# Optimization experiments

Hardware: AMD Instinct MI355X
Metric: run time of the kernel (lower is better)

## Reference

```python
import jax, jax.numpy as jnp
import numpy as np
from jax import lax

D_MODEL=1024; D_STATE=128; D_CONV=4; EXPAND=2; HEADDIM=64
D_INNER=EXPAND*D_MODEL; NHEADS=D_INNER//HEADDIM
POOL=64; SUMDIM=256; TAU1=0.5; TAU2=0.4

def rmsnorm(x, w, eps):
    return x * lax.rsqrt(jnp.mean(x*x, axis=-1, keepdims=True) + eps) * w

def silu(x):
    return x * jax.nn.sigmoid(x)

def setup_inputs():
    key = jax.random.key(0)
    ks = jax.random.split(key, 20)
    B, T = 4, 2048
    d_in_proj = 2*D_INNER + 2*D_STATE + NHEADS
    inp = {
        'x': jax.random.normal(ks[0], (B, T, D_MODEL), jnp.float32),
        'pool': jnp.zeros((B, POOL, SUMDIM), jnp.float32),
        'priorities': jnp.zeros((B, POOL), jnp.float32),
        'counts': jnp.zeros((B,), jnp.int32),
        'norm_w': jnp.ones((D_MODEL,), jnp.float32),
        'in_w': jax.random.normal(ks[1], (d_in_proj, D_MODEL), jnp.float32)*0.02,
        'conv_w': jax.random.normal(ks[2], (D_INNER+2*D_STATE, 1, D_CONV), jnp.float32)*0.1,
        'conv_b': jnp.zeros((D_INNER+2*D_STATE,), jnp.float32),
        'dt_bias': jax.random.uniform(ks[3], (NHEADS,), jnp.float32, -5.0, -1.0),
        'A_log': jnp.log(jax.random.uniform(ks[4], (NHEADS,), jnp.float32, 1.0, 16.0)),
        'Dp': jax.random.normal(ks[5], (NHEADS,), jnp.float32)*0.1 + 1.0,
        'ssm_norm_w': jnp.ones((D_INNER,), jnp.float32),
        'out_w': jax.random.normal(ks[6], (D_MODEL, D_INNER), jnp.float32)*0.02,
        'score_w1': jax.random.normal(ks[7], (D_MODEL//4, D_MODEL), jnp.float32)*0.03,
        'score_w2': jax.random.normal(ks[8], (1, D_MODEL//4), jnp.float32)*0.06,
        'summ_w': jax.random.normal(ks[9], (SUMDIM, D_MODEL), jnp.float32)*0.03,
        'q_w': jax.random.normal(ks[10], (SUMDIM, D_MODEL), jnp.float32)*0.03,
        'k_w': jax.random.normal(ks[11], (SUMDIM, SUMDIM), jnp.float32)*0.06,
        'v_w': jax.random.normal(ks[12], (D_MODEL, SUMDIM), jnp.float32)*0.06,
        'gate_w': jax.random.normal(ks[13], (D_MODEL, 2*D_MODEL), jnp.float32)*0.02,
    }
    return inp

def mamba2(u, in_w, conv_w, conv_b, dt_bias, A_log, Dp, ssm_norm_w, out_w):
    B, T, _ = u.shape
    zxbcdt = u @ in_w.T                      # [B,T,2*d_inner+2*d_state+nheads]
    z = zxbcdt[..., :D_INNER]
    xBC = zxbcdt[..., D_INNER:2*D_INNER+2*D_STATE]
    dt = jax.nn.softplus(zxbcdt[..., 2*D_INNER+2*D_STATE:] + dt_bias)  # [B,T,H]
    # causal depthwise conv over time
    xc = jnp.transpose(xBC, (0, 2, 1))       # [B,C,T]
    xc = lax.conv_general_dilated(xc, conv_w, (1,), [(D_CONV-1, 0)],
                                  dimension_numbers=('NCH', 'OIH', 'NCH'),
                                  feature_group_count=D_INNER+2*D_STATE)
    xBC = silu(jnp.transpose(xc + conv_b[None, :, None], (0, 2, 1)))
    xh = xBC[..., :D_INNER].reshape(B, T, NHEADS, HEADDIM)
    Bm = xBC[..., D_INNER:D_INNER+D_STATE]   # [B,T,N]
    Cm = xBC[..., D_INNER+D_STATE:]          # [B,T,N]
    A = -jnp.exp(A_log)                      # [H]
    dA = jnp.exp(dt * A)                     # [B,T,H]
    def step(h, inp):
        dA_t, dt_t, x_t, B_t, C_t = inp      # [B,H],[B,H],[B,H,P],[B,N],[B,N]
        h = dA_t[:, :, None, None]*h + (dt_t[:, :, None]*x_t)[..., None]*B_t[:, None, None, :]
        y = jnp.einsum('bhpn,bn->bhp', h, C_t)
        return h, y
    h0 = jnp.zeros((B, NHEADS, HEADDIM, D_STATE), u.dtype)
    xs = (jnp.swapaxes(dA, 0, 1), jnp.swapaxes(dt, 0, 1), jnp.swapaxes(xh, 0, 1),
          jnp.swapaxes(Bm, 0, 1), jnp.swapaxes(Cm, 0, 1))
    _, ys = lax.scan(step, h0, xs)           # [T,B,H,P]
    y = jnp.swapaxes(ys, 0, 1) + Dp[None, None, :, None]*xh
    y = y.reshape(B, T, D_INNER)
    y = rmsnorm(y * silu(z), ssm_norm_w, 1e-5)
    return y @ out_w.T

def pool_update(tokens, scores, pool, priorities, counts,
                summ_w):
    B, T, D = tokens.shape
    mask = scores > TAU1
    order = jnp.argsort(-scores, axis=1)     # descending
    s_scores = jnp.take_along_axis(scores, order, 1)
    s_tokens = jnp.take_along_axis(tokens, order[..., None], 1)
    s_mask = jnp.take_along_axis(mask, order, 1)
    summaries = s_tokens @ summ_w.T          # [B,T,SUMDIM]
    nslots = min(T, POOL)
    bidx = jnp.arange(B)
    def slot_step(carry, inp):
        pool, pri, counts = carry
        has_imp, imp, summ = inp             # [B],[B],[B,SUMDIM]
        add = has_imp & (counts < POOL)
        widx = jnp.minimum(counts, POOL-1)
        pool = pool.at[bidx, widx].set(jnp.where(add[:, None], summ, pool[bidx, widx]))
        pri = pri.at[bidx, widx].set(jnp.where(add, imp, pri[bidx, widx]))
        counts = counts + add.astype(counts.dtype)
        replace = has_imp & (counts >= POOL)
        min_idx = jnp.argmin(pri, axis=1)
        min_p = pri[bidx, min_idx]
        should = replace & (imp > min_p)
        pool = pool.at[bidx, min_idx].set(jnp.where(should[:, None], summ, pool[bidx, min_idx]))
        pri = pri.at[bidx, min_idx].set(jnp.where(should, imp, pri[bidx, min_idx]))
        return (pool, pri, counts), None
    xs = (jnp.swapaxes(s_mask[:, :nslots], 0, 1),
          jnp.swapaxes(s_scores[:, :nslots], 0, 1),
          jnp.swapaxes(summaries[:, :nslots], 0, 1))
    (pool, priorities, counts), _ = lax.scan(slot_step, (pool, priorities, counts), xs)
    return pool, priorities, counts

def reference(x, pool, priorities, counts, norm_w, in_w, conv_w, conv_b, dt_bias,
              A_log, Dp, ssm_norm_w, out_w, score_w1, score_w2, summ_w,
              q_w, k_w, v_w, gate_w):
    B = x.shape[0]
    y = x + mamba2(rmsnorm(x, norm_w, 1e-4), in_w, conv_w, conv_b, dt_bias,
                   A_log, Dp, ssm_norm_w, out_w)
    scores = jax.nn.sigmoid(jnp.maximum(y @ score_w1.T, 0.0) @ score_w2.T)[..., 0]
    # layer_idx % cross_layer_frequency == 0 -> update path taken
    pool, priorities, counts = pool_update(y, scores, pool, priorities, counts, summ_w)
    mask = jnp.arange(POOL)[None, :] < counts[:, None]
    q = y @ q_w.T                            # [B,T,S]
    k = pool @ k_w.T                         # [B,P,S]
    v = pool @ v_w.T                         # [B,P,D]
    attn = jnp.einsum('bts,bps->btp', q, k) / (SUMDIM ** 0.5)
    attn = jnp.where(mask[:, None, :], attn, -jnp.inf)
    attn = jnp.nan_to_num(jax.nn.softmax(attn, axis=-1), nan=0.0)
    retrieved = jnp.einsum('btp,bpd->btd', attn, v)
    gate = jax.nn.sigmoid(jnp.concatenate([y, retrieved], axis=-1) @ gate_w.T)
    rmask = ((jnp.mean(scores, axis=1) > TAU2) & (counts > 0)).astype(y.dtype)[:, None, None]
    y = y + gate * retrieved * rmask
    return (y, pool, priorities, counts)
```

## Files before the change

kernel.cpp:

```cpp
#include <hip/hip_runtime.h>


using u16 = unsigned short;
using f16x8 = __attribute__((ext_vector_type(8))) _Float16;
using f32x4  = __attribute__((ext_vector_type(4))) float;

#define DEV __device__ __forceinline__

#define GLOAD4(g, l)  __builtin_amdgcn_global_load_lds((const __attribute__((address_space(1))) void*)(g), (__attribute__((address_space(3))) void*)(l), 4, 0, 0)
#define GLOAD16(g, l) __builtin_amdgcn_global_load_lds((const __attribute__((address_space(1))) void*)(g), (__attribute__((address_space(3))) void*)(l), 16, 0, 0)
#define VMWAIT(N) asm volatile("s_waitcnt vmcnt(" #N ")" ::: "memory")

static constexpr int Bb = 4, T = 2048, D = 1024;
static constexpr int DIN = 2048, DST = 128, NH = 32;
static constexpr int DPROJ = 4384;
static constexpr int CCH = 2304;
static constexpr int ROWS = Bb * T;
static constexpr int NC = 4, CL = 512;
static constexpr float RSC = 4096.f, RSCI = 1.f / 4096.f;

DEV u16 f2h_bits(float f) { union { _Float16 h; u16 u; } v; v.h = (_Float16)f; return v.u; }
DEV float h2f(u16 u) { union { _Float16 h; u16 u; } v; v.u = u; return (float)v.h; }
DEV double sigd(double x) { return 1.0 / (1.0 + exp(-x)); }
DEV int swz(int c) { return c ^ ((c >> 3) & 3); }

__global__ void diag_kernel(float* o, float v) { if (threadIdx.x == 0) o[0] = v; }
__global__ void zerod_kernel(double* p, int n) { if ((int)threadIdx.x < n) p[threadIdx.x] = 0.0; }

__global__ void split2_kernel(const float* __restrict__ in, u16* __restrict__ out, long n) {
    long i = (long)blockIdx.x * 256 + threadIdx.x;
    if (i >= n) return;
    float v = in[i];
    u16 h = f2h_bits(v);
    float r1 = (v - h2f(h)) * RSC;
    out[i] = h;
    out[n + i] = f2h_bits(r1);
}

__global__ __launch_bounds__(256) void rms_x_kernel(const float* __restrict__ x, const float* __restrict__ w,
                                                    u16* __restrict__ up, long pstride) {
    long row = blockIdx.x; int tid = threadIdx.x;
    const float* xr = x + row * D;
    float4 xv = *(const float4*)(xr + tid * 4);
    double ss = (double)xv.x * xv.x + (double)xv.y * xv.y + (double)xv.z * xv.z + (double)xv.w * xv.w;
    for (int off = 1; off < 64; off <<= 1) ss += __shfl_xor(ss, off);
    __shared__ double tmp[4];
    if ((tid & 63) == 0) tmp[tid >> 6] = ss;
    __syncthreads();
    double tot = tmp[0] + tmp[1] + tmp[2] + tmp[3];
    double scale = 1.0 / sqrt(tot / (double)D + 1e-4);
    float4 wv = *(const float4*)(w + tid * 4);
    long base = row * D + tid * 4;
    float vals[4];
    vals[0] = (float)((double)xv.x * scale * (double)wv.x);
    vals[1] = (float)((double)xv.y * scale * (double)wv.y);
    vals[2] = (float)((double)xv.z * scale * (double)wv.z);
    vals[3] = (float)((double)xv.w * scale * (double)wv.w);
#pragma unroll
    for (int j = 0; j < 4; j++) {
        float f = vals[j];
        u16 h = f2h_bits(f);
        up[base + j] = h;
        up[pstride + base + j] = f2h_bits((f - h2f(h)) * RSC);
    }
}

template <int NP>
DEV void stage_one(u16* s0, u16* s1, const float* __restrict__ src, long ld,
                   int row0, int lastrow, int k0, int tid) {
    int r = tid >> 1, cb = (tid & 1) * 2;
    long rg = row0 + r; if (rg > lastrow) rg = lastrow;
    const float* p = src + rg * ld + k0 + cb * 8;
    u16 h16[16], l16[16];
#pragma unroll
    for (int q = 0; q < 4; q++) {
        float4 v4 = *(const float4*)(p + q * 4);
        float vv[4] = { v4.x, v4.y, v4.z, v4.w };
#pragma unroll
        for (int j = 0; j < 4; j++) {
            float xv = vv[j];
            u16 h = f2h_bits(xv);
            h16[q * 4 + j] = h;
            if constexpr (NP == 2) l16[q * 4 + j] = f2h_bits((xv - h2f(h)) * RSC);
        }
    }
    int o0 = swz(r * 4 + cb) * 8, o1 = swz(r * 4 + cb + 1) * 8;
    *(uint4*)(s0 + o0) = *(const uint4*)(h16);
    *(uint4*)(s0 + o1) = *(const uint4*)(h16 + 8);
    if constexpr (NP == 2) {
        *(uint4*)(s1 + o0) = *(const uint4*)(l16);
        *(uint4*)(s1 + o1) = *(const uint4*)(l16 + 8);
    }
}

DEV void stage_pre_dma(u16* dst, const u16* __restrict__ src, long ld,
                       int row0, int lastrow, int k0, int wid, int lane) {
#pragma unroll
    for (int j = 0; j < 2; j++) {
        int s = wid * 128 + j * 64 + lane;
        int g = swz(s);
        int r = g >> 2, cs = g & 3;
        long rg = row0 + r; if (rg > lastrow) rg = lastrow;
        const u16* gp = src + rg * ld + k0 + cs * 8;
        GLOAD16(gp, dst + (wid * 128 + j * 64) * 8);
    }
}

template <int NP, int MODE, bool BP, bool AP>
__global__ __launch_bounds__(256, 2) void gemm_f32(
    const float* __restrict__ A, long lda,
    const u16* __restrict__ Ap, size_t astride,
    const float* __restrict__ B, long ldb,
    const u16* __restrict__ Bp, size_t bstride,
    int M, int N, int K,
    float* __restrict__ out0, float* __restrict__ out1,
    const float* __restrict__ aux0, const float* __restrict__ aux1,
    float* __restrict__ dtb, float* __restrict__ dab) {
    __shared__ __align__(16) u16 sm[NP * 2 * 4096];
    u16* As[2]; u16* Bs[2];
#pragma unroll
    for (int p = 0; p < NP; p++) { As[p] = sm + p * 4096; Bs[p] = sm + (NP + p) * 4096; }
    int tid = threadIdx.x, lane = tid & 63, wid = tid >> 6;
    int wr = wid >> 1, wc = wid & 1;
    int nwg = gridDim.x * gridDim.y;
    int wg = blockIdx.y * gridDim.x + blockIdx.x;
    int lin = (wg & 7) * (nwg >> 3) + (wg >> 3);
    int tM = (lin / gridDim.x) * 128, tN = (lin % gridDim.x) * 128;

    f32x4 acc1[4][4], acc2[4][4];
#pragma unroll
    for (int i = 0; i < 4; i++)
#pragma unroll
        for (int j = 0; j < 4; j++) {
            acc1[i][j] = f32x4{0.f, 0.f, 0.f, 0.f};
            if constexpr (NP == 2) acc2[i][j] = f32x4{0.f, 0.f, 0.f, 0.f};
        }

    int rA = wr * 64 + (lane & 15);
    int rB = wc * 64 + (lane & 15);
    int kc = lane >> 4;
    int oA[4], oB[4];
#pragma unroll
    for (int i = 0; i < 4; i++) {
        oA[i] = swz((rA + i * 16) * 4 + kc) * 8;
        oB[i] = swz((rB + i * 16) * 4 + kc) * 8;
    }

    int nsteps = K / 32;
    for (int kt = 0; kt < nsteps; ++kt) {
        int k0 = kt * 32;
        __syncthreads();
        if constexpr (BP) {
#pragma unroll
            for (int p = 0; p < NP; p++)
                stage_pre_dma(Bs[p], Bp + (size_t)p * bstride, K, tN, N - 1, k0, wid, lane);
        }
        if constexpr (AP) {
#pragma unroll
            for (int p = 0; p < NP; p++)
                stage_pre_dma(As[p], Ap + (size_t)p * astride, K, tM, M - 1, k0, wid, lane);
        } else {
            stage_one<NP>(As[0], NP == 2 ? As[1] : nullptr, A, lda, tM, M - 1, k0, tid);
        }
        if constexpr (!BP) {
            stage_one<NP>(Bs[0], NP == 2 ? Bs[1] : nullptr, B, ldb, tN, N - 1, k0, tid);
        }
        __syncthreads();
        f16x8 fa[4], fb[4];
#pragma unroll
        for (int i = 0; i < 4; i++) {
            fa[i] = *(const f16x8*)(As[0] + oA[i]);
            fb[i] = *(const f16x8*)(Bs[0] + oB[i]);
        }
#pragma unroll
        for (int mi = 0; mi < 4; mi++)
#pragma unroll
            for (int ni = 0; ni < 4; ni++)
                acc1[mi][ni] = __builtin_amdgcn_mfma_f32_16x16x32_f16(fa[mi], fb[ni], acc1[mi][ni], 0, 0, 0);
        if constexpr (NP == 2) {
#pragma unroll
            for (int i = 0; i < 4; i++) fb[i] = *(const f16x8*)(Bs[1] + oB[i]);
#pragma unroll
            for (int mi = 0; mi < 4; mi++)
#pragma unroll
                for (int ni = 0; ni < 4; ni++)
                    acc2[mi][ni] = __builtin_amdgcn_mfma_f32_16x16x32_f16(fa[mi], fb[ni], acc2[mi][ni], 0, 0, 0);
#pragma unroll
            for (int i = 0; i < 4; i++) {
                fa[i] = *(const f16x8*)(As[1] + oA[i]);
                fb[i] = *(const f16x8*)(Bs[0] + oB[i]);
            }
#pragma unroll
            for (int mi = 0; mi < 4; mi++)
#pragma unroll
                for (int ni = 0; ni < 4; ni++)
                    acc2[mi][ni] = __builtin_amdgcn_mfma_f32_16x16x32_f16(fa[mi], fb[ni], acc2[mi][ni], 0, 0, 0);
        }
    }
    int laneh = lane >> 4, lanel = lane & 15;
#pragma unroll
    for (int mi = 0; mi < 4; mi++)
#pragma unroll
        for (int ni = 0; ni < 4; ni++) {
            int col = tN + wc * 64 + ni * 16 + lanel;
            if (col >= N) continue;
#pragma unroll
            for (int r = 0; r < 4; r++) {
                long row = tM + wr * 64 + mi * 16 + laneh * 4 + r;
                float v = acc1[mi][ni][r];
                if constexpr (NP == 2) v += acc2[mi][ni][r] * RSCI;
                if constexpr (MODE == 0) {
                    if (col < 2048) out0[row * 2048 + col] = v;
                    else if (col < 4352) out1[row * 2304 + (col - 2048)] = v;
                    else {
                        int h = col - 4352;
                        double xx = (double)v + (double)aux0[h];
                        double sp = (xx > 30.0) ? xx : log1p(exp(xx));
                        double a = -exp((double)aux1[h]);
                        dtb[row * NH + h] = (float)sp;
                        dab[row * NH + h] = (float)exp(sp * a);
                    }
                } else if constexpr (MODE == 1) {
                    out0[row * 256 + col] = fmaxf(v, 0.f);
                } else if constexpr (MODE == 2) {
                    float y = aux0[row * 1024 + col] + v;
                    out0[row * 1024 + col] = y;
                    out1[row * 2048 + col] = y;
                } else if constexpr (MODE == 3) {
                    out0[row * 256 + col] = v;
                } else {
                    double g = sigd((double)v);
                    float retr = aux0[row * 2048 + 1024 + col];
                    out0[row * 1024 + col] += (float)(g * (double)retr * (double)aux1[row >> 11]);
                }
            }
        }
}

__global__ __launch_bounds__(256) void conv_kernel(const float* __restrict__ xin, const float* __restrict__ cw,
                                                   const float* __restrict__ cb, float* __restrict__ xbc) {
    int blk = blockIdx.x;
    int ct = blk % 36; int tt = (blk / 36) % 32; int b = blk / (36 * 32);
    int c0 = ct * 64, t0 = tt * 64;
    int tid = threadIdx.x;
    __shared__ float tile[67 * 64];
    for (int i = tid; i < 67 * 64; i += 256) {
        int r = i >> 6, c = i & 63;
        int t = t0 - 3 + r;
        tile[i] = (t >= 0) ? xin[((long)(b * T + t)) * CCH + c0 + c] : 0.f;
    }
    __syncthreads();
    int c = tid & 63; int rb = (tid >> 6) * 16;
    int gc = c0 + c;
    double w0 = cw[gc * 4], w1 = cw[gc * 4 + 1], w2 = cw[gc * 4 + 2], w3 = cw[gc * 4 + 3];
    double bias = cb[gc];
    for (int j = 0; j < 16; j++) {
        int tl = rb + j;
        double a = bias + w0 * (double)tile[tl * 64 + c] + w1 * (double)tile[(tl + 1) * 64 + c]
                        + w2 * (double)tile[(tl + 2) * 64 + c] + w3 * (double)tile[(tl + 3) * 64 + c];
        xbc[((long)(b * T + t0 + tl)) * CCH + gc] = (float)(a * sigd(a));
    }
}

#define SCAN_STEP(tt) do { \
    int slot_ = (tt) & 7; \
    float dtv_ = sdt[(tt)], dav_ = sda[(tt)]; \
    float xt0_ = sx[slot_][pp], xt1_ = sx[slot_][pp + 8]; \
    float dtx0_ = dtv_ * xt0_, dtx1_ = dtv_ * xt1_; \
    const float4* BP_ = (const float4*)&sbc[slot_][0]; \
    float y0a_ = 0.f, y0b_ = 0.f, y1a_ = 0.f, y1b_ = 0.f; \
    _Pragma("unroll") \
    for (int r_ = 0; r_ < 4; r_++) { \
        float4 bv_ = BP_[r_ * 8 + sub]; \
        float4 cv_ = BP_[32 + r_ * 8 + sub]; \
        hs0[r_*4+0] = fmaf(dav_, hs0[r_*4+0], dtx0_ * bv_.x); y0a_ = fmaf(hs0[r_*4+0], cv_.x, y0a_); \
        hs0[r_*4+1] = fmaf(dav_, hs0[r_*4+1], dtx0_ * bv_.y); y0b_ = fmaf(hs0[r_*4+1], cv_.y, y0b_); \
        hs0[r_*4+2] = fmaf(dav_, hs0[r_*4+2], dtx0_ * bv_.z); y0a_ = fmaf(hs0[r_*4+2], cv_.z, y0a_); \
        hs0[r_*4+3] = fmaf(dav_, hs0[r_*4+3], dtx0_ * bv_.w); y0b_ = fmaf(hs0[r_*4+3], cv_.w, y0b_); \
        hs1[r_*4+0] = fmaf(dav_, hs1[r_*4+0], dtx1_ * bv_.x); y1a_ = fmaf(hs1[r_*4+0], cv_.x, y1a_); \
        hs1[r_*4+1] = fmaf(dav_, hs1[r_*4+1], dtx1_ * bv_.y); y1b_ = fmaf(hs1[r_*4+1], cv_.y, y1b_); \
        hs1[r_*4+2] = fmaf(dav_, hs1[r_*4+2], dtx1_ * bv_.z); y1a_ = fmaf(hs1[r_*4+2], cv_.z, y1a_); \
        hs1[r_*4+3] = fmaf(dav_, hs1[r_*4+3], dtx1_ * bv_.w); y1b_ = fmaf(hs1[r_*4+3], cv_.w, y1b_); \
    } \
    float y0_ = y0a_ + y0b_, y1_ = y1a_ + y1b_; \
    y0_ += __shfl_xor(y0_, 1); y0_ += __shfl_xor(y0_, 2); y0_ += __shfl_xor(y0_, 4); \
    y1_ += __shfl_xor(y1_, 1); y1_ += __shfl_xor(y1_, 2); y1_ += __shfl_xor(y1_, 4); \
    if (sub == 0) { \
        yout[(long)(tt) * DIN] = y0_ + sDp * xt0_; \
        yout[(long)(tt) * DIN + 8] = y1_ + sDp * xt1_; \
    } \
    runA *= dav_; \
    if (wrc && l == 0) cumAp[(tt)] = runA; \
} while (0)

#define SCAN_ISSUE(s) do { \
    GLOAD16(bcsrc + (long)(s) * CCH, &sbc[(s) & 7][0]); \
    GLOAD4(xsrc + (long)(s) * CCH, &sx[(s) & 7][0]); \
} while (0)

__global__ __launch_bounds__(64) void scan_kernel(const float* __restrict__ xbc, const float* __restrict__ dtb,
                                                  const float* __restrict__ dab, const float* __restrict__ Dp,
                                                  float* __restrict__ ys, float* __restrict__ hend,
                                                  float* __restrict__ cumA) {
    int bx = blockIdx.x;
    int b = bx >> 9, h = (bx >> 4) & 31, c = (bx >> 2) & 3, q4 = bx & 3;
    int l = threadIdx.x;
    int sub = l & 7, pp = l >> 3;
    __shared__ __align__(16) float sbc[8][256];
    __shared__ __align__(16) float sx[8][64];
    __shared__ float sdt[CL];
    __shared__ float sda[CL];
    long rowc = (long)b * T + (long)c * CL;
    const float* bcrow = xbc + rowc * CCH + 2048;
    const float* xrow  = xbc + rowc * CCH + h * 64 + q4 * 16;
    float* yout = ys + rowc * DIN + h * 64 + q4 * 16 + pp;

    int perm = ((l >> 3) & 3) | ((l & 7) << 2) | (l & 32);
    const float* bcsrc = bcrow + perm * 4;
    const float* xsrc  = xrow + (l & 15);

    bool wrc = (q4 == 0);
    float* cumAp = cumA + ((long)(b * 32 + h)) * T + (long)c * CL;
    float runA = 1.f;

    for (int i = 0; i < CL / 64; i++) {
        GLOAD4(dtb + (rowc + i * 64 + l) * NH + h, &sdt[i * 64]);
        GLOAD4(dab + (rowc + i * 64 + l) * NH + h, &sda[i * 64]);
    }
#pragma unroll
    for (int s = 0; s < 6; s++) SCAN_ISSUE(s);

    float hs0[16], hs1[16];
#pragma unroll
    for (int j = 0; j < 16; j++) { hs0[j] = 0.f; hs1[j] = 0.f; }
    float sDp = Dp[h];

    constexpr int NI = CL / 2;
    for (int i = 0; i < NI - 3; i++) {
        int s0 = 2 * i + 6;
        SCAN_ISSUE(s0);
        SCAN_ISSUE(s0 + 1);
        VMWAIT(12);
        __builtin_amdgcn_sched_barrier(0);
        SCAN_STEP(2 * i);
        SCAN_STEP(2 * i + 1);
    }
    { int i = NI - 3; VMWAIT(8); __builtin_amdgcn_sched_barrier(0); SCAN_STEP(2 * i); SCAN_STEP(2 * i + 1); }
    { int i = NI - 2; VMWAIT(4); __builtin_amdgcn_sched_barrier(0); SCAN_STEP(2 * i); SCAN_STEP(2 * i + 1); }
    { int i = NI - 1; VMWAIT(0); __builtin_amdgcn_sched_barrier(0); SCAN_STEP(2 * i); SCAN_STEP(2 * i + 1); }

    if (c < NC - 1) {
        float* hp = hend + (((long)(b * 32 + h)) * (NC - 1) + c) * 8192 + (q4 * 16 + pp) * 128 + sub * 16;
#pragma unroll
        for (int j = 0; j < 16; j += 4) *(float4*)(hp + j) = *(float4*)&hs0[j];
        float* hp1 = hp + 8 * 128;
#pragma unroll
        for (int j = 0; j < 16; j += 4) *(float4*)(hp1 + j) = *(float4*)&hs1[j];
    }
}

__global__ __launch_bounds__(256) void scanfix_kernel(float* __restrict__ hend, const float* __restrict__ cumA) {
    int bh = blockIdx.x; int tid = threadIdx.x;
    float P1 = cumA[(long)bh * T + 2 * CL - 1];
    float P2 = cumA[(long)bh * T + 3 * CL - 1];
    float* h0 = hend + (long)bh * (NC - 1) * 8192;
    float* h1 = h0 + 8192;
    float* h2 = h1 + 8192;
    for (int e = tid; e < 8192; e += 256) {
        float a = h0[e];
        float b2 = fmaf(P1, a, h1[e]); h1[e] = b2;
        h2[e] = fmaf(P2, b2, h2[e]);
    }
}

__global__ __launch_bounds__(256) void scancorr_kernel(const float* __restrict__ hend, const float* __restrict__ cumA,
                                                       const float* __restrict__ xbc, float* __restrict__ ys) {
    int blk = blockIdx.x;
    int tq = blk & 3;
    int cm = (blk >> 2) % 3;
    int bh = blk / 12;
    int b = bh >> 5, h = bh & 31;
    int tid = threadIdx.x;
    int p = tid >> 2, nq = tid & 3;
    const float* Hin = hend + ((long)bh * (NC - 1) + cm) * 8192 + p * 128 + nq * 32;
    float hreg[32];
#pragma unroll
    for (int j = 0; j < 32; j += 4) *(float4*)&hreg[j] = *(const float4*)(Hin + j);
    __shared__ float sC[8][128];
    long t0 = (long)(cm + 1) * CL + tq * 128;
    const float* cA = cumA + (long)bh * T;
    for (int tg = 0; tg < 16; tg++) {
        __syncthreads();
        {
            int tt = tg * 8 + (tid >> 5);
            int cc = (tid & 31) * 4;
            *(float4*)&sC[tid >> 5][cc] = *(const float4*)(xbc + ((long)b * T + t0 + tt) * CCH + 2176 + cc);
        }
        __syncthreads();
#pragma unroll
        for (int j = 0; j < 8; j++) {
            long t = t0 + tg * 8 + j;
            const float* Cr = &sC[j][nq * 32];
            float d = 0.f;
#pragma unroll
            for (int k = 0; k < 32; k += 4) {
                float4 cv = *(const float4*)(Cr + k);
                d += hreg[k] * cv.x + hreg[k + 1] * cv.y + hreg[k + 2] * cv.z + hreg[k + 3] * cv.w;
            }
            d += __shfl_xor(d, 1);
            d += __shfl_xor(d, 2);
            if (nq == 0) {
                float ca = cA[t];
                ys[((long)b * T + t) * DIN + h * 64 + p] += ca * d;
            }
        }
    }
}

__global__ __launch_bounds__(256) void ssmnorm_kernel(float* __restrict__ ys, const float* __restrict__ z,
                                                      const float* __restrict__ w) {
    long row = blockIdx.x; int tid = threadIdx.x;
    float* yr = ys + row * DIN;
    const float* zr = z + row * DIN;
    double v[8]; double ss = 0.0;
#pragma unroll
    for (int j = 0; j < 8; j++) {
        int c = tid * 8 + j;
        double zz = (double)zr[c];
        double val = (double)yr[c] * (zz * sigd(zz));
        v[j] = val; ss += val * val;
    }
    for (int off = 1; off < 64; off <<= 1) ss += __shfl_xor(ss, off);
    __shared__ double tmp[4];
    if ((tid & 63) == 0) tmp[tid >> 6] = ss;
    __syncthreads();
    double tot = tmp[0] + tmp[1] + tmp[2] + tmp[3];
    double scale = 1.0 / sqrt(tot / (double)DIN + 1e-5);
#pragma unroll
    for (int j = 0; j < 8; j++) {
        int c = tid * 8 + j;
        yr[c] = (float)(v[j] * scale * (double)w[c]);
    }
}

__global__ void score2_kernel(const float* __restrict__ sh, const float* __restrict__ w2,
                              float* __restrict__ scores, double* __restrict__ ssum) {
    int row = blockIdx.x * 4 + (threadIdx.x >> 6);
    int lane = threadIdx.x & 63;
    const float* h = sh + (long)row * 256;
    double a = 0.0;
    for (int j = 0; j < 4; j++) a += (double)h[lane * 4 + j] * (double)w2[lane * 4 + j];
    for (int off = 1; off < 64; off <<= 1) a += __shfl_xor(a, off);
    if (lane == 0) {
        double sc = sigd(a);
        scores[row] = (float)sc;
        atomicAdd(&ssum[row >> 11], sc);
    }
}

__global__ void top64_kernel(const float* __restrict__ scores, int* __restrict__ tidx, float* __restrict__ tval) {
    int b = blockIdx.x; int tid = threadIdx.x;
    __shared__ float s[T];
    __shared__ float rv[256];
    __shared__ int ri[256];
    for (int i = tid; i < T; i += 256) s[i] = scores[b * T + i];
    for (int k = 0; k < 64; k++) {
        __syncthreads();
        float best = -1e30f; int bi = 1 << 30;
        for (int i = tid; i < T; i += 256) {
            float v = s[i];
            if (v > best || (v == best && i < bi)) { best = v; bi = i; }
        }
        rv[tid] = best; ri[tid] = bi;
        __syncthreads();
        for (int off = 128; off > 0; off >>= 1) {
            if (tid < off) {
                float v2 = rv[tid + off]; int i2 = ri[tid + off];
                if (v2 > rv[tid] || (v2 == rv[tid] && i2 < ri[tid])) { rv[tid] = v2; ri[tid] = i2; }
            }
            __syncthreads();
        }
        if (tid == 0) { tidx[b * 64 + k] = ri[0]; tval[b * 64 + k] = rv[0]; s[ri[0]] = -1e30f; }
    }
}

__global__ __launch_bounds__(256) void summ_kernel(const float* __restrict__ y, const int* __restrict__ tidx,
                                                   const float* __restrict__ wsum, float* __restrict__ summ) {
    int s = blockIdx.x & 63; int b = blockIdx.x >> 6;
    int tid = threadIdx.x;
    __shared__ float yrow[1024];
    int tok = tidx[b * 64 + s];
    long base = ((long)(b * T + tok));
    for (int i = tid; i < 1024; i += 256) yrow[i] = y[base * 1024 + i];
    __syncthreads();
    double acc = 0.0;
    const float* w = wsum + (long)tid * 1024;
    for (int kk = 0; kk < 1024; kk++) acc += (double)yrow[kk] * (double)w[kk];
    summ[((long)(b * 64 + s)) * 256 + tid] = (float)acc;
}

__global__ void pool_kernel(const float* __restrict__ pin, const float* __restrict__ prin,
                            const int* __restrict__ cin, const float* __restrict__ tval,
                            const float* __restrict__ summ, const double* __restrict__ ssum,
                            float* __restrict__ pout, float* __restrict__ prout,
                            float* __restrict__ cout, float* __restrict__ rmask) {
    int b = blockIdx.x; int tid = threadIdx.x;
    __shared__ float spri[64];
    __shared__ int scount, sact, sslot, srep, srslot;
    for (int i = tid; i < 64 * 256; i += 256) pout[(long)b * 16384 + i] = pin[(long)b * 16384 + i];
    if (tid < 64) spri[tid] = prin[b * 64 + tid];
    if (tid == 0) scount = cin[b];
    __syncthreads();
    for (int s = 0; s < 64; s++) {
        float imp = tval[b * 64 + s];
        bool has = imp > 0.5f;
        if (tid == 0) {
            sact = 0;
            if (has && scount < 64) { sslot = scount; spri[scount] = imp; scount++; sact = 1; }
        }
        __syncthreads();
        if (sact) pout[((long)(b * 64 + sslot)) * 256 + tid] = summ[((long)(b * 64 + s)) * 256 + tid];
        if (tid < 64) {
            float v = spri[tid]; int idx = tid;
            for (int off = 1; off < 64; off <<= 1) {
                float v2 = __shfl_xor(v, off); int i2 = __shfl_xor(idx, off);
                if (v2 < v || (v2 == v && i2 < idx)) { v = v2; idx = i2; }
            }
            if (tid == 0) {
                srep = 0;
                if (has && scount >= 64 && imp > v) { srep = 1; srslot = idx; spri[idx] = imp; }
            }
        }
        __syncthreads();
        if (srep) pout[((long)(b * 64 + srslot)) * 256 + tid] = summ[((long)(b * 64 + s)) * 256 + tid];
        __syncthreads();
    }
    if (tid < 64) prout[b * 64 + tid] = spri[tid];
    if (tid == 0) {
        cout[b] = (float)scount;
        double mean = ssum[b] / (double)T;
        rmask[b] = (mean > 0.4 && scount > 0) ? 1.f : 0.f;
    }
}

__global__ __launch_bounds__(256) void kv_kernel(const float* __restrict__ pool, const float* __restrict__ kw,
                                                 const float* __restrict__ vw, float* __restrict__ k,
                                                 float* __restrict__ v) {
    int blk = blockIdx.x; int b = blk >> 6, s = blk & 63; int tid = threadIdx.x;
    __shared__ float pr[256];
    pr[tid] = pool[((long)(b * 64 + s)) * 256 + tid];
    __syncthreads();
    float a = 0.f;
    const float* w = kw + (long)tid * 256;
    for (int j = 0; j < 256; j++) a = fmaf(pr[j], w[j], a);
    k[((long)(b * 64 + s)) * 256 + tid] = a;
    for (int m = 0; m < 4; m++) {
        int o = m * 256 + tid;
        const float* w2 = vw + (long)o * 256;
        float c = 0.f;
        for (int j = 0; j < 256; j++) c = fmaf(pr[j], w2[j], c);
        v[((long)(b * 64 + s)) * 1024 + o] = c;
    }
}

__global__ __launch_bounds__(256) void attn_kernel(const float* __restrict__ q, const float* __restrict__ k,
                                                   const float* __restrict__ v, const float* __restrict__ cout,
                                                   float* __restrict__ concat) {
    long row = blockIdx.x;
    int b = (int)(row >> 11);
    int tid = threadIdx.x;
    int cnt = (int)cout[b];
    __shared__ float qs[256], slog[64], sp[64];
    qs[tid] = q[row * 256 + tid];
    __syncthreads();
    int s = tid >> 2, part = tid & 3;
    const float* kr = k + ((long)(b * 64 + s)) * 256 + part * 64;
    float d = 0.f;
    for (int j = 0; j < 64; j++) d = fmaf(qs[part * 64 + j], kr[j], d);
    d += __shfl_xor(d, 1); d += __shfl_xor(d, 2);
    if (part == 0) slog[s] = d * 0.0625f;
    __syncthreads();
    if (tid < 64) {
        float l = (tid < cnt) ? slog[tid] : -1e30f;
        float m = l;
        for (int off = 1; off < 64; off <<= 1) m = fmaxf(m, __shfl_xor(m, off));
        float e = (tid < cnt) ? expf(l - m) : 0.f;
        float su = e;
        for (int off = 1; off < 64; off <<= 1) su += __shfl_xor(su, off);
        sp[tid] = (cnt > 0) ? e / su : 0.f;
    }
    __syncthreads();
    float acc[4] = {0.f, 0.f, 0.f, 0.f};
    for (int s2 = 0; s2 < cnt; s2++) {
        float p = sp[s2];
        const float* vr = v + ((long)(b * 64 + s2)) * 1024 + tid;
        acc[0] = fmaf(p, vr[0], acc[0]);
        acc[1] = fmaf(p, vr[256], acc[1]);
        acc[2] = fmaf(p, vr[512], acc[2]);
        acc[3] = fmaf(p, vr[768], acc[3]);
    }
    for (int j = 0; j < 4; j++) concat[row * 2048 + 1024 + tid + j * 256] = acc[j];
}

extern "C" void kernel_launch(void* const* d_in, const int* in_sizes, int n_in,
                              void* d_out, int out_size, void* d_ws, size_t ws_size,
                              hipStream_t stream) {
    (void)in_sizes; (void)n_in; (void)out_size;
    const float* x       = (const float*)d_in[0];
    const float* pool_in = (const float*)d_in[1];
    const float* pri_in  = (const float*)d_in[2];
    const int*   cnt_in  = (const int*)d_in[3];
    const float* norm_w  = (const float*)d_in[4];
    const float* in_w    = (const float*)d_in[5];
    const float* conv_w  = (const float*)d_in[6];
    const float* conv_b  = (const float*)d_in[7];
    const float* dt_bias = (const float*)d_in[8];
    const float* A_log   = (const float*)d_in[9];
    const float* Dp      = (const float*)d_in[10];
    const float* ssm_w   = (const float*)d_in[11];
    const float* out_w   = (const float*)d_in[12];
    const float* s_w1    = (const float*)d_in[13];
    const float* s_w2    = (const float*)d_in[14];
    const float* summ_w  = (const float*)d_in[15];
    const float* q_w     = (const float*)d_in[16];
    const float* k_w     = (const float*)d_in[17];
    const float* v_w     = (const float*)d_in[18];
    const float* gate_w  = (const float*)d_in[19];

    float* outy    = (float*)d_out;
    float* outpool = outy + (long)ROWS * D;
    float* outpri  = outpool + Bb * 64 * 256;
    float* outcnt  = outpri + Bb * 64;

    char* ws = (char*)d_ws;
    size_t cur = 0;
    auto alloc = [&](size_t bytes) { size_t o = cur; cur += (bytes + 255) / 256 * 256; return o; };

    size_t pw_in_bytes   = (size_t)2 * DPROJ * 1024 * 2;
    size_t ra_bytes = (size_t)ROWS * CCH * 4;

    size_t o_dt   = alloc((size_t)ROWS * NH * 4);
    size_t o_da   = alloc((size_t)ROWS * NH * 4);
    size_t o_sc   = alloc((size_t)ROWS * 4);
    size_t o_ssum = alloc(64);
    size_t o_rmk  = alloc(64);
    size_t o_tidx = alloc(Bb * 64 * 4);
    size_t o_tval = alloc(Bb * 64 * 4);
    size_t o_summ = alloc((size_t)Bb * 64 * 256 * 4);
    size_t o_k    = alloc((size_t)Bb * 64 * 256 * 4);
    size_t o_v    = alloc((size_t)Bb * 64 * 1024 * 4);
    size_t o_hend = alloc((size_t)128 * (NC - 1) * 8192 * 4);
    size_t o_cumA = alloc((size_t)128 * T * 4);
    size_t o_RA = alloc(ra_bytes);
    size_t o_RB = alloc((size_t)ROWS * DIN * 4);
    size_t o_RC = alloc((size_t)ROWS * CCH * 4);

    if (ws_size < cur) {
        diag_kernel<<<1, 64, 0, stream>>>(outy, 1000.0f + (float)(ws_size >> 20));
        return;
    }

    float* dtb    = (float*)(ws + o_dt);
    float* dab    = (float*)(ws + o_da);
    float* scores = (float*)(ws + o_sc);
    double* ssum  = (double*)(ws + o_ssum);
    float* rmk    = (float*)(ws + o_rmk);
    int*   tidx   = (int*)(ws + o_tidx);
    float* tval   = (float*)(ws + o_tval);
    float* summ   = (float*)(ws + o_summ);
    float* kbuf   = (float*)(ws + o_k);
    float* vbuf   = (float*)(ws + o_v);
    float* hend   = (float*)(ws + o_hend);
    float* cumA   = (float*)(ws + o_cumA);

    u16*  pw_in   = (u16*)(ws + o_RA);
    u16*  uplanes = (u16*)(ws + o_RA + pw_in_bytes);
    float* xbc    = (float*)(ws + o_RA);
    float* concat = (float*)(ws + o_RA);
    float* sch    = (float*)(ws + o_RA + (size_t)ROWS * DIN * 4);
    float* bufZ   = (float*)(ws + o_RB);
    u16*  pw_out  = (u16*)(ws + o_RB);
    u16*  pw_s1   = (u16*)(ws + o_RB + (size_t)16 * 1024 * 1024);
    float* qbuf   = (float*)(ws + o_RB);
    float* bufX   = (float*)(ws + o_RC);
    float* yscan  = (float*)(ws + o_RC);

    zerod_kernel<<<1, 64, 0, stream>>>(ssum, 4);
    {
        long n = (long)DPROJ * 1024;
        split2_kernel<<<(n + 255) / 256, 256, 0, stream>>>(in_w, pw_in, n);
    }
    rms_x_kernel<<<ROWS, 256, 0, stream>>>(x, norm_w, uplanes, (long)ROWS * D);
    gemm_f32<2, 0, true, true><<<dim3(35, 64), 256, 0, stream>>>(
        nullptr, 0, uplanes, (size_t)ROWS * D,
        nullptr, 0, pw_in, (size_t)DPROJ * 1024,
        ROWS, DPROJ, 1024,
        bufZ, bufX, dt_bias, A_log, dtb, dab);
    conv_kernel<<<Bb * 32 * 36, 256, 0, stream>>>(bufX, conv_w, conv_b, xbc);
    scan_kernel<<<Bb * NH * NC * 4, 64, 0, stream>>>(xbc, dtb, dab, Dp, yscan, hend, cumA);
    scanfix_kernel<<<128, 256, 0, stream>>>(hend, cumA);
    scancorr_kernel<<<128 * 3 * 4, 256, 0, stream>>>(hend, cumA, xbc, yscan);
    ssmnorm_kernel<<<ROWS, 256, 0, stream>>>(yscan, bufZ, ssm_w);
    {
        long n = (long)1024 * 2048;
        split2_kernel<<<(n + 255) / 256, 256, 0, stream>>>(out_w, pw_out, n);
        long n2 = (long)256 * 1024;
        split2_kernel<<<(n2 + 255) / 256, 256, 0, stream>>>(s_w1, pw_s1, n2);
    }
    gemm_f32<2, 2, true, false><<<dim3(8, 64), 256, 0, stream>>>(
        yscan, 2048, nullptr, 0,
        nullptr, 0, pw_out, (size_t)1024 * 2048,
        ROWS, 1024, 2048,
        outy, concat, x, nullptr, nullptr, nullptr);
    gemm_f32<2, 1, true, false><<<dim3(2, 64), 256, 0, stream>>>(
        outy, 1024, nullptr, 0,
        nullptr, 0, pw_s1, (size_t)256 * 1024,
        ROWS, 256, 1024,
        sch, nullptr, nullptr, nullptr, nullptr, nullptr);
    score2_kernel<<<ROWS / 4, 256, 0, stream>>>(sch, s_w2, scores, ssum);
    top64_kernel<<<Bb, 256, 0, stream>>>(scores, tidx, tval);
    summ_kernel<<<Bb * 64, 256, 0, stream>>>(outy, tidx, summ_w, summ);
    pool_kernel<<<Bb, 256, 0, stream>>>(pool_in, pri_in, cnt_in, tval, summ, ssum,
                                        outpool, outpri, outcnt, rmk);
    kv_kernel<<<Bb * 64, 256, 0, stream>>>(outpool, k_w, v_w, kbuf, vbuf);
    gemm_f32<1, 3, false, false><<<dim3(2, 64), 256, 0, stream>>>(
        outy, 1024, nullptr, 0,
        q_w, 1024, nullptr, 0,
        ROWS, 256, 1024,
        qbuf, nullptr, nullptr, nullptr, nullptr, nullptr);
    attn_kernel<<<ROWS, 256, 0, stream>>>(qbuf, kbuf, vbuf, outcnt, concat);
    gemm_f32<1, 4, false, false><<<dim3(8, 64), 256, 0, stream>>>(
        concat, 2048, nullptr, 0,
        gate_w, 2048, nullptr, 0,
        ROWS, 1024, 2048,
        outy, nullptr, concat, rmk, nullptr, nullptr);
}
```

Baseline: 1.734 ms.

## Double-buffer LDS tiles in GEMM and drop scan sched barriers

The GEMM kernel now holds two LDS tile buffers. It stages the next K-tile while running MFMAs on the current one, and needs only one barrier per iteration instead of two. The goal is to hide global-to-LDS load latency behind compute. The cost is double the LDS footprint per workgroup, which can limit occupancy at two blocks per CU. Separately, the scan loop drops its sched_barrier calls, so the compiler is free to interleave the scan steps with the wait instructions.

```diff
diff --git a/kernel.cpp b/kernel.cpp
--- a/kernel.cpp
+++ b/kernel.cpp
@@ -105,6 +105,26 @@
         GLOAD16(gp, dst + (wid * 128 + j * 64) * 8);
     }
 }
+
+#define STAGE_TILE(bb, k0_) do { \
+    u16* As0_ = (bb); \
+    u16* As1_ = (bb) + 4096; \
+    u16* Bs0_ = (bb) + NP * 4096; \
+    u16* Bs1_ = (bb) + NP * 4096 + 4096; \
+    if constexpr (BP) { \
+        stage_pre_dma(Bs0_, Bp, K, tN, N - 1, (k0_), wid, lane); \
+        if constexpr (NP == 2) stage_pre_dma(Bs1_, Bp + bstride, K, tN, N - 1, (k0_), wid, lane); \
+    } \
+    if constexpr (AP) { \
+        stage_pre_dma(As0_, Ap, K, tM, M - 1, (k0_), wid, lane); \
+        if constexpr (NP == 2) stage_pre_dma(As1_, Ap + astride, K, tM, M - 1, (k0_), wid, lane); \
+    } else { \
+        stage_one<NP>(As0_, NP == 2 ? As1_ : nullptr, A, lda, tM, M - 1, (k0_), tid); \
+    } \
+    if constexpr (!BP) { \
+        stage_one<NP>(Bs0_, NP == 2 ? Bs1_ : nullptr, B, ldb, tN, N - 1, (k0_), tid); \
+    } \
+} while (0)
 
 template <int NP, int MODE, bool BP, bool AP>
 __global__ __launch_bounds__(256, 2) void gemm_f32(
@@ -116,10 +136,7 @@
     float* __restrict__ out0, float* __restrict__ out1,
     const float* __restrict__ aux0, const float* __restrict__ aux1,
     float* __restrict__ dtb, float* __restrict__ dab) {
-    __shared__ __align__(16) u16 sm[NP * 2 * 4096];
-    u16* As[2]; u16* Bs[2];
-#pragma unroll
-    for (int p = 0; p < NP; p++) { As[p] = sm + p * 4096; Bs[p] = sm + (NP + p) * 4096; }
+    __shared__ __align__(16) u16 sm[2 * NP * 2 * 4096];
     int tid = threadIdx.x, lane = tid & 63, wid = tid >> 6;
     int wr = wid >> 1, wc = wid & 1;
     int nwg = gridDim.x * gridDim.y;
@@ -147,30 +164,22 @@
     }
 
     int nsteps = K / 32;
+    int cur = 0;
+    STAGE_TILE(sm, 0);
+    __syncthreads();
     for (int kt = 0; kt < nsteps; ++kt) {
-        int k0 = kt * 32;
-        __syncthreads();
-        if constexpr (BP) {
-#pragma unroll
-            for (int p = 0; p < NP; p++)
-                stage_pre_dma(Bs[p], Bp + (size_t)p * bstride, K, tN, N - 1, k0, wid, lane);
-        }
-        if constexpr (AP) {
-#pragma unroll
-            for (int p = 0; p < NP; p++)
-                stage_pre_dma(As[p], Ap + (size_t)p * astride, K, tM, M - 1, k0, wid, lane);
-        } else {
-            stage_one<NP>(As[0], NP == 2 ? As[1] : nullptr, A, lda, tM, M - 1, k0, tid);
-        }
-        if constexpr (!BP) {
-            stage_one<NP>(Bs[0], NP == 2 ? Bs[1] : nullptr, B, ldb, tN, N - 1, k0, tid);
-        }
-        __syncthreads();
+        u16* cb = sm + cur * (NP * 2 * 4096);
+        if (kt + 1 < nsteps) {
+            u16* nb = sm + (cur ^ 1) * (NP * 2 * 4096);
+            STAGE_TILE(nb, (kt + 1) * 32);
+        }
+        u16* As0 = cb; u16* As1 = cb + 4096;
+        u16* Bs0 = cb + NP * 4096; u16* Bs1 = cb + NP * 4096 + 4096;
         f16x8 fa[4], fb[4];
 #pragma unroll
         for (int i = 0; i < 4; i++) {
-            fa[i] = *(const f16x8*)(As[0] + oA[i]);
-            fb[i] = *(const f16x8*)(Bs[0] + oB[i]);
+            fa[i] = *(const f16x8*)(As0 + oA[i]);
+            fb[i] = *(const f16x8*)(Bs0 + oB[i]);
         }
 #pragma unroll
         for (int mi = 0; mi < 4; mi++)
@@ -179,7 +188,7 @@
                 acc1[mi][ni] = __builtin_amdgcn_mfma_f32_16x16x32_f16(fa[mi], fb[ni], acc1[mi][ni], 0, 0, 0);
         if constexpr (NP == 2) {
 #pragma unroll
-            for (int i = 0; i < 4; i++) fb[i] = *(const f16x8*)(Bs[1] + oB[i]);
+            for (int i = 0; i < 4; i++) fb[i] = *(const f16x8*)(Bs1 + oB[i]);
 #pragma unroll
             for (int mi = 0; mi < 4; mi++)
 #pragma unroll
@@ -187,14 +196,18 @@
                     acc2[mi][ni] = __builtin_amdgcn_mfma_f32_16x16x32_f16(fa[mi], fb[ni], acc2[mi][ni], 0, 0, 0);
 #pragma unroll
             for (int i = 0; i < 4; i++) {
-                fa[i] = *(const f16x8*)(As[1] + oA[i]);
-                fb[i] = *(const f16x8*)(Bs[0] + oB[i]);
+                fa[i] = *(const f16x8*)(As1 + oA[i]);
+                fb[i] = *(const f16x8*)(Bs0 + oB[i]);
             }
 #pragma unroll
             for (int mi = 0; mi < 4; mi++)
 #pragma unroll
                 for (int ni = 0; ni < 4; ni++)
                     acc2[mi][ni] = __builtin_amdgcn_mfma_f32_16x16x32_f16(fa[mi], fb[ni], acc2[mi][ni], 0, 0, 0);
+        }
+        if (kt + 1 < nsteps) {
+            __syncthreads();
+            cur ^= 1;
         }
     }
     int laneh = lane >> 4, lanel = lane & 15;
@@ -341,13 +354,12 @@
         SCAN_ISSUE(s0);
         SCAN_ISSUE(s0 + 1);
         VMWAIT(12);
-        __builtin_amdgcn_sched_barrier(0);
         SCAN_STEP(2 * i);
         SCAN_STEP(2 * i + 1);
     }
-    { int i = NI - 3; VMWAIT(8); __builtin_amdgcn_sched_barrier(0); SCAN_STEP(2 * i); SCAN_STEP(2 * i + 1); }
-    { int i = NI - 2; VMWAIT(4); __builtin_amdgcn_sched_barrier(0); SCAN_STEP(2 * i); SCAN_STEP(2 * i + 1); }
-    { int i = NI - 1; VMWAIT(0); __builtin_amdgcn_sched_barrier(0); SCAN_STEP(2 * i); SCAN_STEP(2 * i + 1); }
+    { int i = NI - 3; VMWAIT(8); SCAN_STEP(2 * i); SCAN_STEP(2 * i + 1); }
+    { int i = NI - 2; VMWAIT(4); SCAN_STEP(2 * i); SCAN_STEP(2 * i + 1); }
+    { int i = NI - 1; VMWAIT(0); SCAN_STEP(2 * i); SCAN_STEP(2 * i + 1); }
 
     if (c < NC - 1) {
         float* hp = hend + (((long)(b * 32 + h)) * (NC - 1) + c) * 8192 + (q4 * 16 + pp) * 128 + sub * 16;
```

Measured after the change: 1.709 ms. About the same (-1.5%).
